# Kernel tuning notes

Measured on AMD Instinct MI355X. Metric: run time of the kernel, lower is better.

The kernel has to match this reference:

```python
import jax, jax.numpy as jnp
import numpy as np

N_NODES = 50000
N_EDGES = 640000
D_IN = 128
D_HID = 256
D_OUT = 128


def _linear_params(key, d_in, d_out):
    kw, kb = jax.random.split(key)
    bound = 1.0 / np.sqrt(d_in)
    W = jax.random.uniform(kw, (d_in, d_out), jnp.float32, -bound, bound)
    b = jax.random.uniform(kb, (d_out,), jnp.float32, -bound, bound)
    return W, b


def setup_inputs() -> dict:
    key = jax.random.key(0)
    ks = jax.random.split(key, 6)
    x = jax.random.normal(ks[0], (N_NODES, D_IN), jnp.float32)
    edge_index = jax.random.randint(ks[1], (2, N_EDGES), 0, N_NODES, jnp.int64)
    W1a, b1a = _linear_params(ks[2], D_IN, D_HID)
    W1b, b1b = _linear_params(ks[3], D_HID, D_HID)
    W2a, b2a = _linear_params(ks[4], D_HID, D_HID)
    W2b, b2b = _linear_params(ks[5], D_HID, D_OUT)
    return {"x": x, "edge_index": edge_index,
            "W1a": W1a, "b1a": b1a, "W1b": W1b, "b1b": b1b,
            "W2a": W2a, "b2a": b2a, "W2b": W2b, "b2b": b2b}


def _gin_conv(x, src, dst, Wa, ba, Wb, bb):
    # sum-aggregate neighbor features: agg[i] = sum_{(j->i) in E} x[j]
    agg = jax.ops.segment_sum(x[src], dst, num_segments=N_NODES)
    h = x + agg  # (1 + eps) * x + agg, eps = 0 (PyG default)
    h = jnp.maximum(h @ Wa + ba, 0.0)  # Linear + ReLU
    return h @ Wb + bb                 # Linear


def reference(x, edge_index, W1a, b1a, W1b, b1b, W2a, b2a, W2b, b2b):
    src, dst = edge_index[0], edge_index[1]
    h = _gin_conv(x, src, dst, W1a, b1a, W1b, b1b)
    h = jnp.maximum(h, 0.0)  # ReLU; dropout is identity in eval mode
    return _gin_conv(h, src, dst, W2a, b2a, W2b, b2b)
```

## Files before the change

### kernel.cpp

```cpp
#include <hip/hip_runtime.h>

#define N_NODES 50000
#define N_EDGES 640000
#define PADROWS 50048
#define SLOTS   48

typedef __attribute__((ext_vector_type(8))) short bf16x8;
typedef __attribute__((ext_vector_type(4))) float f32x4;

__device__ inline ushort rne16(float f) {
    unsigned u = __builtin_bit_cast(unsigned, f);
    unsigned r = u + 0x7fffu + ((u >> 16) & 1u);
    return (ushort)(r >> 16);
}
__device__ inline float b2f(ushort h) {
    return __builtin_bit_cast(float, (unsigned)h << 16);
}

__device__ inline void glds16(const ushort* g, ushort* l) {
    __builtin_amdgcn_global_load_lds(
        (const __attribute__((address_space(1))) void*)g,
        (__attribute__((address_space(3))) void*)l, 16, 0, 0);
}

#define EB  ((N_EDGES + 255) / 256)
#define RB  ((N_NODES * 128 / 4 + 255) / 256)

__global__ __launch_bounds__(256) void prep_kernel(const int* __restrict__ src,
                                                   const int* __restrict__ dst,
                                                   int* __restrict__ cnt,
                                                   int* __restrict__ elist,
                                                   const float* __restrict__ W1a,
                                                   const float* __restrict__ W1b,
                                                   const float* __restrict__ W2a,
                                                   const float* __restrict__ W2b,
                                                   ushort* __restrict__ o1a,
                                                   ushort* __restrict__ o1b,
                                                   ushort* __restrict__ o2a,
                                                   ushort* __restrict__ o2b,
                                                   const float* __restrict__ x,
                                                   ushort* __restrict__ xb) {
    int blk = blockIdx.x;
    if (blk < EB) {
        int e = blk * 256 + threadIdx.x;
        if (e < N_EDGES) {
            unsigned d = (unsigned)dst[e];
            unsigned s = (unsigned)src[e];
            if (d < N_NODES && s < N_NODES) {
                int pos = atomicAdd(&cnt[d], 1);
                if (pos < SLOTS) elist[(size_t)d * SLOTS + pos] = (int)s;
            }
        }
        return;
    }
    blk -= EB;
    if (blk < 768) {
        const float* W; ushort* O; int K, N, base;
        if (blk < 128)      { W = W1a; O = o1a; K = 128; N = 256; base = 0; }
        else if (blk < 384) { W = W1b; O = o1b; K = 256; N = 256; base = 128; }
        else if (blk < 640) { W = W2a; O = o2a; K = 256; N = 256; base = 384; }
        else                { W = W2b; O = o2b; K = 256; N = 128; base = 640; }
        int idx = (blk - base) * 256 + threadIdx.x;
        int n = idx / K, k = idx - n * K;
        O[idx] = rne16(W[(size_t)k * N + n]);
        return;
    }
    blk -= 768;
    int i = blk * 256 + threadIdx.x;
    if (i < N_NODES * 128 / 4) {
        float4 v = ((const float4*)x)[i];
        ushort4 o = make_ushort4(rne16(v.x), rne16(v.y), rne16(v.z), rne16(v.w));
        ((ushort4*)xb)[i] = o;
    }
}

__global__ __launch_bounds__(256) void agg_x(const float* __restrict__ x,
                                             const ushort* __restrict__ xb,
                                             const int* __restrict__ cnt,
                                             const int* __restrict__ elist,
                                             ushort* __restrict__ h0b) {
    const int l = threadIdx.x & 31;
    const int node = blockIdx.x * 8 + (threadIdx.x >> 5);
    if (node >= N_NODES) return;
    float4 s4 = ((const float4*)(x + (size_t)node * 128))[l];
    float a0 = s4.x, a1 = s4.y, a2 = s4.z, a3 = s4.w;
    float c0 = 0.f, c1 = 0.f, c2 = 0.f, c3 = 0.f;
    int n = cnt[node]; if (n > SLOTS) n = SLOTS;
    const int* el = elist + (size_t)node * SLOTS;
    int i = 0;
    for (; i + 2 <= n; i += 2) {
        ushort4 v0 = ((const ushort4*)(xb + (size_t)el[i] * 128))[l];
        ushort4 v1 = ((const ushort4*)(xb + (size_t)el[i + 1] * 128))[l];
        a0 += b2f(v0.x); a1 += b2f(v0.y); a2 += b2f(v0.z); a3 += b2f(v0.w);
        c0 += b2f(v1.x); c1 += b2f(v1.y); c2 += b2f(v1.z); c3 += b2f(v1.w);
    }
    if (i < n) {
        ushort4 v = ((const ushort4*)(xb + (size_t)el[i] * 128))[l];
        a0 += b2f(v.x); a1 += b2f(v.y); a2 += b2f(v.z); a3 += b2f(v.w);
    }
    a0 += c0; a1 += c1; a2 += c2; a3 += c3;
    ushort4 o = make_ushort4(rne16(a0), rne16(a1), rne16(a2), rne16(a3));
    ((ushort4*)(h0b + (size_t)node * 128))[l] = o;
}

__global__ __launch_bounds__(256) void agg_h(const ushort* __restrict__ hBb,
                                             const int* __restrict__ cnt,
                                             const int* __restrict__ elist,
                                             ushort* __restrict__ hCb) {
    const int l = threadIdx.x & 63;
    const int node = blockIdx.x * 4 + (threadIdx.x >> 6);
    if (node >= N_NODES) return;
    ushort4 s4 = ((const ushort4*)(hBb + (size_t)node * 256))[l];
    float a0 = b2f(s4.x), a1 = b2f(s4.y), a2 = b2f(s4.z), a3 = b2f(s4.w);
    float c0 = 0.f, c1 = 0.f, c2 = 0.f, c3 = 0.f;
    int n = cnt[node]; if (n > SLOTS) n = SLOTS;
    const int* el = elist + (size_t)node * SLOTS;
    int i = 0;
    for (; i + 2 <= n; i += 2) {
        ushort4 v0 = ((const ushort4*)(hBb + (size_t)el[i] * 256))[l];
        ushort4 v1 = ((const ushort4*)(hBb + (size_t)el[i + 1] * 256))[l];
        a0 += b2f(v0.x); a1 += b2f(v0.y); a2 += b2f(v0.z); a3 += b2f(v0.w);
        c0 += b2f(v1.x); c1 += b2f(v1.y); c2 += b2f(v1.z); c3 += b2f(v1.w);
    }
    if (i < n) {
        ushort4 v = ((const ushort4*)(hBb + (size_t)el[i] * 256))[l];
        a0 += b2f(v.x); a1 += b2f(v.y); a2 += b2f(v.z); a3 += b2f(v.w);
    }
    a0 += c0; a1 += c1; a2 += c2; a3 += c3;
    ushort4 o = make_ushort4(rne16(a0), rne16(a1), rne16(a2), rne16(a3));
    ((ushort4*)(hCb + (size_t)node * 256))[l] = o;
}


template <int K1, int N2, bool RELU2, bool BF16OUT>
__global__ __launch_bounds__(256, 2) void fused_mlp(const ushort* __restrict__ Ag,
                                                    const ushort* __restrict__ W1g,
                                                    const float* __restrict__ b1,
                                                    const ushort* __restrict__ W2g,
                                                    const float* __restrict__ b2,
                                                    float* __restrict__ Cf,
                                                    ushort* __restrict__ Cb,
                                                    int M) {
    constexpr int NI2 = N2 / 32;
    __shared__ ushort bufA[64 * 64];
    __shared__ ushort bufB[256 * 64];
    __shared__ ushort C1[64 * 256];
    const int tid = threadIdx.x;
    const int lane = tid & 63;
    const int wid = tid >> 6;
    const int wm = wid >> 1, wn = wid & 1;
    const int row0 = blockIdx.x * 64;
    const int stB = lane >> 3;
    const int kel = (((lane & 7) << 4) ^ (stB << 4)) >> 1;

    f32x4 acc1[2][8];
#pragma unroll
    for (int i = 0; i < 2; ++i)
#pragma unroll
        for (int j = 0; j < 8; ++j) acc1[i][j] = (f32x4){0.f, 0.f, 0.f, 0.f};

    for (int k0 = 0; k0 < K1; k0 += 64) {
#pragma unroll
        for (int i = 0; i < 10; ++i) {
            int t = i * 4 + wid;
            if (t < 8) glds16(Ag + (size_t)(row0 + t * 8 + stB) * K1 + k0 + kel, bufA + t * 512);
            else       glds16(W1g + (size_t)((t - 8) * 8 + stB) * K1 + k0 + kel, bufB + (t - 8) * 512);
        }
        __syncthreads();
#pragma unroll
        for (int ki = 0; ki < 2; ++ki) {
            const int kb = ki * 64 + ((lane >> 4) << 4);
            bf16x8 a[2], b[8];
#pragma unroll
            for (int mi = 0; mi < 2; ++mi) {
                int row = wm * 32 + mi * 16 + (lane & 15);
                int off = (row * 128 + kb) ^ ((row & 7) << 4);
                a[mi] = *(const bf16x8*)((const char*)bufA + off);
            }
#pragma unroll
            for (int ni = 0; ni < 8; ++ni) {
                int col = wn * 128 + ni * 16 + (lane & 15);
                int off = (col * 128 + kb) ^ ((col & 7) << 4);
                b[ni] = *(const bf16x8*)((const char*)bufB + off);
            }
#pragma unroll
            for (int mi = 0; mi < 2; ++mi)
#pragma unroll
                for (int ni = 0; ni < 8; ++ni)
                    acc1[mi][ni] = __builtin_amdgcn_mfma_f32_16x16x32_bf16(a[mi], b[ni], acc1[mi][ni], 0, 0, 0);
        }
        __syncthreads();
    }
#pragma unroll
    for (int ni = 0; ni < 8; ++ni) {
        int col = wn * 128 + ni * 16 + (lane & 15);
        float bv = b1[col];
#pragma unroll
        for (int mi = 0; mi < 2; ++mi) {
            int rowb = wm * 32 + mi * 16 + ((lane >> 4) << 2);
            f32x4 av = acc1[mi][ni];
#pragma unroll
            for (int r = 0; r < 4; ++r) {
                int row = rowb + r;
                int off = (row * 512 + col * 2) ^ ((row & 7) << 4);
                *(ushort*)((char*)C1 + off) = rne16(fmaxf(av[r] + bv, 0.f));
            }
        }
    }

    f32x4 acc2[2][NI2];
#pragma unroll
    for (int i = 0; i < 2; ++i)
#pragma unroll
        for (int j = 0; j < NI2; ++j) acc2[i][j] = (f32x4){0.f, 0.f, 0.f, 0.f};

    for (int k0 = 0; k0 < 256; k0 += 64) {
#pragma unroll
        for (int i = 0; i < N2 / 32; ++i) {
            int t = i * 4 + wid;
            glds16(W2g + (size_t)(t * 8 + stB) * 256 + k0 + kel, bufB + t * 512);
        }
        __syncthreads();
#pragma unroll
        for (int ki = 0; ki < 2; ++ki) {
            const int kb = ki * 64 + ((lane >> 4) << 4);
            bf16x8 a[2], b[NI2];
#pragma unroll
            for (int mi = 0; mi < 2; ++mi) {
                int row = wm * 32 + mi * 16 + (lane & 15);
                int off = (row * 512 + k0 * 2 + kb) ^ ((row & 7) << 4);
                a[mi] = *(const bf16x8*)((const char*)C1 + off);
            }
#pragma unroll
            for (int ni = 0; ni < NI2; ++ni) {
                int col = wn * (N2 / 2) + ni * 16 + (lane & 15);
                int off = (col * 128 + kb) ^ ((col & 7) << 4);
                b[ni] = *(const bf16x8*)((const char*)bufB + off);
            }
#pragma unroll
            for (int mi = 0; mi < 2; ++mi)
#pragma unroll
                for (int ni = 0; ni < NI2; ++ni)
                    acc2[mi][ni] = __builtin_amdgcn_mfma_f32_16x16x32_bf16(a[mi], b[ni], acc2[mi][ni], 0, 0, 0);
        }
        __syncthreads();
    }
#pragma unroll
    for (int ni = 0; ni < NI2; ++ni) {
        int col = wn * (N2 / 2) + ni * 16 + (lane & 15);
        float bv = b2[col];
#pragma unroll
        for (int mi = 0; mi < 2; ++mi) {
            int rowb = row0 + wm * 32 + mi * 16 + ((lane >> 4) << 2);
            f32x4 av = acc2[mi][ni];
#pragma unroll
            for (int r = 0; r < 4; ++r) {
                int row = rowb + r;
                if (row < M) {
                    float f = av[r] + bv;
                    if (RELU2) f = fmaxf(f, 0.f);
                    if (BF16OUT) Cb[(size_t)row * N2 + col] = rne16(f);
                    else         Cf[(size_t)row * N2 + col] = f;
                }
            }
        }
    }
}


extern "C" void kernel_launch(void* const* d_in, const int* in_sizes, int n_in,
                              void* d_out, int out_size, void* d_ws, size_t ws_size,
                              hipStream_t stream) {
    const float* x   = (const float*)d_in[0];
    const int*   ei  = (const int*)d_in[1];
    const float* W1a = (const float*)d_in[2];
    const float* b1a = (const float*)d_in[3];
    const float* W1b = (const float*)d_in[4];
    const float* b1b = (const float*)d_in[5];
    const float* W2a = (const float*)d_in[6];
    const float* b2a = (const float*)d_in[7];
    const float* W2b = (const float*)d_in[8];
    const float* b2b = (const float*)d_in[9];
    float* out = (float*)d_out;

    const int* src = ei;
    const int* dst = ei + N_EDGES;

    int* cnt   = (int*)d_ws;
    int* elist = cnt + N_NODES;

    size_t ob = (((size_t)(N_NODES + (size_t)N_NODES * SLOTS) * 4) + 255) & ~(size_t)255;
    ushort* w1a = (ushort*)((char*)d_ws + ob);
    ushort* w1b = w1a + 256 * 128;
    ushort* w2a = w1b + 256 * 256;
    ushort* w2b = w2a + 256 * 256;
    char*   wend = (char*)(w2b + 128 * 256);

    size_t fb = ((size_t)(wend - (char*)d_ws) + 255) & ~(size_t)255;
    const size_t P128 = (size_t)PADROWS * 128;
    const size_t P256 = (size_t)PADROWS * 256;
    ushort* xb  = (ushort*)((char*)d_ws + fb);
    ushort* h0b = xb  + P128;
    ushort* hBb = h0b + P128;
    ushort* hCb = hBb + P256;

    hipMemsetAsync(cnt, 0, (size_t)N_NODES * sizeof(int), stream);

    prep_kernel<<<EB + 768 + RB, 256, 0, stream>>>(
        src, dst, cnt, elist, W1a, W1b, W2a, W2b, w1a, w1b, w2a, w2b, x, xb);

    const int gb = PADROWS / 64;
    agg_x<<<(N_NODES + 7) / 8, 256, 0, stream>>>(x, xb, cnt, elist, h0b);
    fused_mlp<128, 256, true, true><<<gb, 256, 0, stream>>>(
        h0b, w1a, b1a, w1b, b1b, nullptr, hBb, N_NODES);
    agg_h<<<(N_NODES + 3) / 4, 256, 0, stream>>>(hBb, cnt, elist, hCb);
    fused_mlp<256, 128, false, false><<<gb, 256, 0, stream>>>(
        hCb, w2a, b2a, w2b, b2b, out, nullptr, N_NODES);
}
```

Baseline: 197.2 us.

## Compress edge lists to 16-bit, tile weight transpose, use bf16 self term

Edge slot lists now hold 16-bit node indices instead of 32-bit, which halves their footprint and the index traffic in both aggregation kernels. The weight transpose and bf16 conversion now goes through a padded 32x32 shared-memory tile, so global reads and writes are coalesced and far fewer blocks are launched. The first aggregation reads the self feature from the bf16 copy instead of fp32, which cuts bytes but adds a small rounding change. Node IDs must stay below 65536; this holds for 50000 nodes but is not a general solution.

```diff
diff --git a/kernel.cpp b/kernel.cpp
--- a/kernel.cpp
+++ b/kernel.cpp
@@ -29,7 +29,7 @@
 __global__ __launch_bounds__(256) void prep_kernel(const int* __restrict__ src,
                                                    const int* __restrict__ dst,
                                                    int* __restrict__ cnt,
-                                                   int* __restrict__ elist,
+                                                   ushort* __restrict__ elist,
                                                    const float* __restrict__ W1a,
                                                    const float* __restrict__ W1b,
                                                    const float* __restrict__ W2a,
@@ -40,6 +40,7 @@
                                                    ushort* __restrict__ o2b,
                                                    const float* __restrict__ x,
                                                    ushort* __restrict__ xb) {
+    __shared__ float tileLds[32][33];
     int blk = blockIdx.x;
     if (blk < EB) {
         int e = blk * 256 + threadIdx.x;
@@ -48,24 +49,36 @@
             unsigned s = (unsigned)src[e];
             if (d < N_NODES && s < N_NODES) {
                 int pos = atomicAdd(&cnt[d], 1);
-                if (pos < SLOTS) elist[(size_t)d * SLOTS + pos] = (int)s;
+                if (pos < SLOTS) elist[(size_t)d * SLOTS + pos] = (ushort)s;
             }
         }
         return;
     }
     blk -= EB;
-    if (blk < 768) {
-        const float* W; ushort* O; int K, N, base;
-        if (blk < 128)      { W = W1a; O = o1a; K = 128; N = 256; base = 0; }
-        else if (blk < 384) { W = W1b; O = o1b; K = 256; N = 256; base = 128; }
-        else if (blk < 640) { W = W2a; O = o2a; K = 256; N = 256; base = 384; }
-        else                { W = W2b; O = o2b; K = 256; N = 128; base = 640; }
-        int idx = (blk - base) * 256 + threadIdx.x;
-        int n = idx / K, k = idx - n * K;
-        O[idx] = rne16(W[(size_t)k * N + n]);
+    if (blk < 192) {
+        const float* W; ushort* O; int K, N, tbase;
+        if (blk < 32)       { W = W1a; O = o1a; K = 128; N = 256; tbase = 0; }
+        else if (blk < 96)  { W = W1b; O = o1b; K = 256; N = 256; tbase = 32; }
+        else if (blk < 160) { W = W2a; O = o2a; K = 256; N = 256; tbase = 96; }
+        else                { W = W2b; O = o2b; K = 256; N = 128; tbase = 160; }
+        int tile = blk - tbase;
+        int nt = N >> 5;
+        int tk = tile / nt, tn = tile % nt;
+        int cc = threadIdx.x & 31, rr0 = threadIdx.x >> 5;
+#pragma unroll
+        for (int it = 0; it < 4; ++it) {
+            int r = rr0 + it * 8;
+            tileLds[r][cc] = W[(size_t)(tk * 32 + r) * N + tn * 32 + cc];
+        }
+        __syncthreads();
+#pragma unroll
+        for (int it = 0; it < 4; ++it) {
+            int r = rr0 + it * 8;
+            O[(size_t)(tn * 32 + r) * K + tk * 32 + cc] = rne16(tileLds[cc][r]);
+        }
         return;
     }
-    blk -= 768;
+    blk -= 192;
     int i = blk * 256 + threadIdx.x;
     if (i < N_NODES * 128 / 4) {
         float4 v = ((const float4*)x)[i];
@@ -74,23 +87,23 @@
     }
 }
 
-__global__ __launch_bounds__(256) void agg_x(const float* __restrict__ x,
-                                             const ushort* __restrict__ xb,
+__global__ __launch_bounds__(256) void agg_x(const ushort* __restrict__ xb,
                                              const int* __restrict__ cnt,
-                                             const int* __restrict__ elist,
+                                             const ushort* __restrict__ elist,
                                              ushort* __restrict__ h0b) {
     const int l = threadIdx.x & 31;
     const int node = blockIdx.x * 8 + (threadIdx.x >> 5);
     if (node >= N_NODES) return;
-    float4 s4 = ((const float4*)(x + (size_t)node * 128))[l];
-    float a0 = s4.x, a1 = s4.y, a2 = s4.z, a3 = s4.w;
+    ushort4 s4 = ((const ushort4*)(xb + (size_t)node * 128))[l];
+    float a0 = b2f(s4.x), a1 = b2f(s4.y), a2 = b2f(s4.z), a3 = b2f(s4.w);
     float c0 = 0.f, c1 = 0.f, c2 = 0.f, c3 = 0.f;
     int n = cnt[node]; if (n > SLOTS) n = SLOTS;
-    const int* el = elist + (size_t)node * SLOTS;
+    const ushort* el = elist + (size_t)node * SLOTS;
     int i = 0;
     for (; i + 2 <= n; i += 2) {
-        ushort4 v0 = ((const ushort4*)(xb + (size_t)el[i] * 128))[l];
-        ushort4 v1 = ((const ushort4*)(xb + (size_t)el[i + 1] * 128))[l];
+        int s0 = el[i], s1 = el[i + 1];
+        ushort4 v0 = ((const ushort4*)(xb + (size_t)s0 * 128))[l];
+        ushort4 v1 = ((const ushort4*)(xb + (size_t)s1 * 128))[l];
         a0 += b2f(v0.x); a1 += b2f(v0.y); a2 += b2f(v0.z); a3 += b2f(v0.w);
         c0 += b2f(v1.x); c1 += b2f(v1.y); c2 += b2f(v1.z); c3 += b2f(v1.w);
     }
@@ -105,7 +118,7 @@
 
 __global__ __launch_bounds__(256) void agg_h(const ushort* __restrict__ hBb,
                                              const int* __restrict__ cnt,
-                                             const int* __restrict__ elist,
+                                             const ushort* __restrict__ elist,
                                              ushort* __restrict__ hCb) {
     const int l = threadIdx.x & 63;
     const int node = blockIdx.x * 4 + (threadIdx.x >> 6);
@@ -114,11 +127,12 @@
     float a0 = b2f(s4.x), a1 = b2f(s4.y), a2 = b2f(s4.z), a3 = b2f(s4.w);
     float c0 = 0.f, c1 = 0.f, c2 = 0.f, c3 = 0.f;
     int n = cnt[node]; if (n > SLOTS) n = SLOTS;
-    const int* el = elist + (size_t)node * SLOTS;
+    const ushort* el = elist + (size_t)node * SLOTS;
     int i = 0;
     for (; i + 2 <= n; i += 2) {
-        ushort4 v0 = ((const ushort4*)(hBb + (size_t)el[i] * 256))[l];
-        ushort4 v1 = ((const ushort4*)(hBb + (size_t)el[i + 1] * 256))[l];
+        int s0 = el[i], s1 = el[i + 1];
+        ushort4 v0 = ((const ushort4*)(hBb + (size_t)s0 * 256))[l];
+        ushort4 v1 = ((const ushort4*)(hBb + (size_t)s1 * 256))[l];
         a0 += b2f(v0.x); a1 += b2f(v0.y); a2 += b2f(v0.z); a3 += b2f(v0.w);
         c0 += b2f(v1.x); c1 += b2f(v1.y); c2 += b2f(v1.z); c3 += b2f(v1.w);
     }
@@ -286,10 +300,10 @@
     const int* src = ei;
     const int* dst = ei + N_EDGES;
 
-    int* cnt   = (int*)d_ws;
-    int* elist = cnt + N_NODES;
-
-    size_t ob = (((size_t)(N_NODES + (size_t)N_NODES * SLOTS) * 4) + 255) & ~(size_t)255;
+    int* cnt      = (int*)d_ws;
+    ushort* elist = (ushort*)(cnt + N_NODES);
+
+    size_t ob = (((size_t)N_NODES * 4 + (size_t)N_NODES * SLOTS * 2) + 255) & ~(size_t)255;
     ushort* w1a = (ushort*)((char*)d_ws + ob);
     ushort* w1b = w1a + 256 * 128;
     ushort* w2a = w1b + 256 * 256;
@@ -306,11 +320,11 @@
 
     hipMemsetAsync(cnt, 0, (size_t)N_NODES * sizeof(int), stream);
 
-    prep_kernel<<<EB + 768 + RB, 256, 0, stream>>>(
+    prep_kernel<<<EB + 192 + RB, 256, 0, stream>>>(
         src, dst, cnt, elist, W1a, W1b, W2a, W2b, w1a, w1b, w2a, w2b, x, xb);
 
     const int gb = PADROWS / 64;
-    agg_x<<<(N_NODES + 7) / 8, 256, 0, stream>>>(x, xb, cnt, elist, h0b);
+    agg_x<<<(N_NODES + 7) / 8, 256, 0, stream>>>(xb, cnt, elist, h0b);
     fused_mlp<128, 256, true, true><<<gb, 256, 0, stream>>>(
         h0b, w1a, b1a, w1b, b1b, nullptr, hBb, N_NODES);
     agg_h<<<(N_NODES + 3) / 4, 256, 0, stream>>>(hBb, cnt, elist, hCb);
```

Result: no change. 194.0 us (-1.6%).
